# Optimization experiments

Measured on AMD Instinct MI355X. Metric: run time of the kernel, lower is better.

Reference implementation:

```python
import jax, jax.numpy as jnp
import numpy as np

N = 100000      # nodes
E = 1600000     # edges
G = 4096        # graphs (molecules)
F_NODE, F_MOL = 64, 128
EN, D0, D1, D2, D3, OUT = 64, 128, 128, 256, 64, 1
EPS_BN = 1e-5


def setup_inputs() -> dict:
    key = jax.random.key(0)
    ks = iter(jax.random.split(key, 40))
    def w(shape, scale=0.1):
        return jax.random.normal(next(ks), shape, dtype=jnp.float32) * scale
    inp = {
        "x": jax.random.normal(next(ks), (N, F_NODE), dtype=jnp.float32),
        "atom_ens": jax.random.uniform(next(ks), (N,), dtype=jnp.float32),
        "mol_feats": jax.random.normal(next(ks), (G, F_MOL), dtype=jnp.float32),
        "edge_index": jax.random.randint(next(ks), (2, E), 0, N, dtype=jnp.int32),
        "batch": jnp.sort(jax.random.randint(next(ks), (N,), 0, G, dtype=jnp.int32)),
        # electronegativity embedding
        "W_en": w((F_NODE, EN)), "b_en": w((EN,)),
        # GCN layers
        "gW0": w((EN, D0)), "gb0": w((D0,)),
        "gW1": w((D0, D0)), "gb1": w((D0,)),
        "gW2": w((D0, D1)), "gb2": w((D1,)),
        "bn_gc_g": jnp.ones((D0,), jnp.float32), "bn_gc_b": jnp.zeros((D0,), jnp.float32),
        # mol-feature MLP branch
        "mW0": w((F_MOL, D0)), "mb0": w((D0,)),
        "mW1": w((D0, D0)), "mb1": w((D0,)),
        "mW2": w((D0, D1)), "mb2": w((D1,)),
        "bn_m_g": jnp.ones((D0,), jnp.float32), "bn_m_b": jnp.zeros((D0,), jnp.float32),
        # fused head
        "fW0": w((2 * D1, D2)), "fb0": w((D2,)),
        "fW1": w((D2, D2)), "fb1": w((D2,)),
        "fW2": w((D2, D3)), "fb2": w((D3,)),
        "fW3": w((D3, OUT)), "fb3": w((OUT,)),
    }
    return inp


def _bn(x, gamma, beta):
    # BatchNorm1d in training mode: batch stats, biased variance
    mu = jnp.mean(x, axis=0)
    var = jnp.mean(jnp.square(x - mu), axis=0)
    return (x - mu) * jax.lax.rsqrt(var + EPS_BN) * gamma + beta


def reference(x, atom_ens, mol_feats, edge_index, batch,
              W_en, b_en,
              gW0, gb0, gW1, gb1, gW2, gb2, bn_gc_g, bn_gc_b,
              mW0, mb0, mW1, mb1, mW2, mb2, bn_m_g, bn_m_b,
              fW0, fb0, fW1, fb1, fW2, fb2, fW3, fb3):
    silu = jax.nn.silu
    # GCN normalization with self-loops (PyG gcn_norm), shared by all layers
    loop = jnp.arange(N, dtype=edge_index.dtype)
    src = jnp.concatenate([edge_index[0], loop])   # [E+N]
    dst = jnp.concatenate([edge_index[1], loop])
    deg = jax.ops.segment_sum(jnp.ones_like(dst, x.dtype), dst, num_segments=N)
    dinv = jax.lax.rsqrt(deg)                      # deg >= 1 due to self-loops
    norm = dinv[src] * dinv[dst]                   # [E+N]

    def gcn(h, W, b):
        h = h @ W                                  # transform then propagate
        msg = h[src] * norm[:, None]               # gather + scale
        return jax.ops.segment_sum(msg, dst, num_segments=N) + b

    # calc_en: linear -> L2 normalize per node -> scale by atom electronegativity
    fo = x @ W_en + b_en
    fo = fo / jnp.maximum(jnp.linalg.norm(fo, axis=1, keepdims=True), 1e-12)
    en = atom_ens[:, None] * fo

    h = silu(_bn(gcn(en, gW0, gb0), bn_gc_g, bn_gc_b))
    h = silu(gcn(h, gW1, gb1))
    h = silu(gcn(h, gW2, gb2))
    hg = jax.ops.segment_sum(h, batch, num_segments=G)   # global_add_pool

    hm = silu(_bn(mol_feats @ mW0 + mb0, bn_m_g, bn_m_b))
    hm = silu(hm @ mW1 + mb1)
    hm = silu(hm @ mW2 + mb2)

    hg = jnp.concatenate([hg, hm], axis=1)
    hg = silu(hg @ fW0 + fb0)
    hg = silu(hg @ fW1 + fb1)
    hg = silu(hg @ fW2 + fb2)
    return hg @ fW3 + fb3
```

## Files before the change

### kernel.cpp

```cpp
#include <hip/hip_runtime.h>
#include <math.h>

static __device__ __forceinline__ float silu_f(float v){ return v/(1.0f+expf(-v)); }
static __device__ __forceinline__ unsigned short f2bf(float f){
  unsigned int u=__float_as_uint(f);
  unsigned int r=(u + 0x7fffu + ((u>>16)&1u))>>16;
  return (unsigned short)r;
}
static __device__ __forceinline__ void bf2f(unsigned int u, float& a, float& b){
  a=__uint_as_float(u<<16); b=__uint_as_float(u & 0xffff0000u);
}

__global__ void k_hist(const int* __restrict__ dst, int* __restrict__ cnt, int E){
  int e = blockIdx.x*256+threadIdx.x;
  if(e<E) atomicAdd(&cnt[dst[e]],1);
}
__global__ void k_dinv(const int* __restrict__ cnt, float* __restrict__ dinv, int n){
  int i = blockIdx.x*256+threadIdx.x;
  if(i<n) dinv[i]=rsqrtf((float)(cnt[i]+1));
}
__global__ void k_scan1(const int* __restrict__ cnt, int* __restrict__ rp, int* __restrict__ bs, int n){
  __shared__ int sh[256];
  int tid=threadIdx.x;
  int base = blockIdx.x*1024 + tid*4;
  int v0=0,v1=0,v2=0,v3=0;
  if(base+0<n)v0=cnt[base+0];
  if(base+1<n)v1=cnt[base+1];
  if(base+2<n)v2=cnt[base+2];
  if(base+3<n)v3=cnt[base+3];
  int s=v0+v1+v2+v3;
  sh[tid]=s; __syncthreads();
  for(int off=1;off<256;off<<=1){
    int t = (tid>=off)? sh[tid-off] : 0;
    __syncthreads();
    sh[tid]+=t;
    __syncthreads();
  }
  int run = sh[tid]-s;
  if(tid==255) bs[blockIdx.x]=sh[255];
  if(base+0<n){rp[base+0]=run; run+=v0;}
  if(base+1<n){rp[base+1]=run; run+=v1;}
  if(base+2<n){rp[base+2]=run; run+=v2;}
  if(base+3<n){rp[base+3]=run; run+=v3;}
}
__global__ void k_scan2(int* bs, int nb, int* rp, int n){
  __shared__ int sh[256];
  int tid=threadIdx.x;
  int v = (tid<nb)? bs[tid] : 0;
  sh[tid]=v; __syncthreads();
  for(int off=1;off<256;off<<=1){
    int t=(tid>=off)?sh[tid-off]:0;
    __syncthreads();
    sh[tid]+=t;
    __syncthreads();
  }
  if(tid<nb) bs[tid]=sh[tid]-v;
  if(tid==255) rp[n]=sh[255];
}
__global__ void k_scan3(int* rp, const int* __restrict__ bs, int n){
  int i = blockIdx.x*256+threadIdx.x;
  if(i<n) rp[i]+=bs[i>>10];
}
__global__ void k_fill(const int* __restrict__ src, const int* __restrict__ dst, int* cur,
                       const int* __restrict__ rp, int* __restrict__ csr, int E){
  int e = blockIdx.x*256+threadIdx.x;
  if(e<E){ int d=dst[e]; int p=atomicAdd(&cur[d],1); csr[rp[d]+p]=src[e]; }
}

__global__ __launch_bounds__(256) void k_en(const float* __restrict__ x, const float* __restrict__ W,
    const float* __restrict__ b, const float* __restrict__ ae, unsigned short* __restrict__ out, int Nn){
  __shared__ float As[32][68];
  __shared__ float Bs[32][68];
  int bm = blockIdx.x*64;
  int tid = threadIdx.x;
  int ty = tid/16, tx = tid%16;
  float acc[4][4] = {{0}};
  for(int k0=0;k0<64;k0+=32){
    #pragma unroll
    for(int i=0;i<8;i++){
      int idx = i*256+tid;
      int r = idx>>5, c = idx&31;
      As[c][r] = (bm+r<Nn) ? x[(size_t)(bm+r)*64 + k0+c] : 0.0f;
    }
    #pragma unroll
    for(int i=0;i<8;i++){
      int idx = i*256+tid;
      int r = idx>>6, c = idx&63;
      Bs[r][c] = W[(size_t)(k0+r)*64 + c];
    }
    __syncthreads();
    #pragma unroll
    for(int k=0;k<32;k++){
      float a0=As[k][ty*4+0],a1=As[k][ty*4+1],a2=As[k][ty*4+2],a3=As[k][ty*4+3];
      float b0=Bs[k][tx*4+0],b1=Bs[k][tx*4+1],b2=Bs[k][tx*4+2],b3=Bs[k][tx*4+3];
      acc[0][0]+=a0*b0; acc[0][1]+=a0*b1; acc[0][2]+=a0*b2; acc[0][3]+=a0*b3;
      acc[1][0]+=a1*b0; acc[1][1]+=a1*b1; acc[1][2]+=a1*b2; acc[1][3]+=a1*b3;
      acc[2][0]+=a2*b0; acc[2][1]+=a2*b1; acc[2][2]+=a2*b2; acc[2][3]+=a2*b3;
      acc[3][0]+=a3*b0; acc[3][1]+=a3*b1; acc[3][2]+=a3*b2; acc[3][3]+=a3*b3;
    }
    __syncthreads();
  }
  float bb0=b[tx*4+0], bb1=b[tx*4+1], bb2=b[tx*4+2], bb3=b[tx*4+3];
  #pragma unroll
  for(int i=0;i<4;i++){
    int row = bm+ty*4+i;
    float v0=acc[i][0]+bb0, v1=acc[i][1]+bb1, v2=acc[i][2]+bb2, v3=acc[i][3]+bb3;
    float ss = v0*v0+v1*v1+v2*v2+v3*v3;
    ss += __shfl_xor(ss,1); ss += __shfl_xor(ss,2);
    ss += __shfl_xor(ss,4); ss += __shfl_xor(ss,8);
    if(row<Nn){
      float scale = ae[row] / fmaxf(sqrtf(ss), 1e-12f);
      ushort4 o;
      o.x=f2bf(v0*scale); o.y=f2bf(v1*scale); o.z=f2bf(v2*scale); o.w=f2bf(v3*scale);
      *(ushort4*)&out[(size_t)row*64 + tx*4] = o;
    }
  }
}

template<int FB>
__global__ __launch_bounds__(256) void k_prop_bf(const unsigned short* __restrict__ h, float* __restrict__ out,
                       const int* __restrict__ rp, const int* __restrict__ csr,
                       const float* __restrict__ dinv, int Nn){
  int t = blockIdx.x*256+threadIdx.x;
  int n = t/FB;
  if(n>=Nn) return;
  int g = (t%FB)*8;
  const int F = FB*8;
  float dn = dinv[n];
  float a0,a1,a2,a3,a4,a5,a6,a7;
  {
    uint4 u = *(const uint4*)&h[(size_t)n*F+g];
    bf2f(u.x,a0,a1); bf2f(u.y,a2,a3); bf2f(u.z,a4,a5); bf2f(u.w,a6,a7);
    a0*=dn;a1*=dn;a2*=dn;a3*=dn;a4*=dn;a5*=dn;a6*=dn;a7*=dn;
  }
  int e=rp[n], e1=rp[n+1];
  for(; e+1<e1; e+=2){
    int s0=csr[e], s1=csr[e+1];
    float w0=dinv[s0], w1=dinv[s1];
    uint4 u0 = *(const uint4*)&h[(size_t)s0*F+g];
    uint4 u1 = *(const uint4*)&h[(size_t)s1*F+g];
    float b0,b1,b2,b3,b4,b5,b6,b7;
    bf2f(u0.x,b0,b1); bf2f(u0.y,b2,b3); bf2f(u0.z,b4,b5); bf2f(u0.w,b6,b7);
    a0+=b0*w0; a1+=b1*w0; a2+=b2*w0; a3+=b3*w0;
    a4+=b4*w0; a5+=b5*w0; a6+=b6*w0; a7+=b7*w0;
    bf2f(u1.x,b0,b1); bf2f(u1.y,b2,b3); bf2f(u1.z,b4,b5); bf2f(u1.w,b6,b7);
    a0+=b0*w1; a1+=b1*w1; a2+=b2*w1; a3+=b3*w1;
    a4+=b4*w1; a5+=b5*w1; a6+=b6*w1; a7+=b7*w1;
  }
  if(e<e1){
    int s=csr[e]; float w=dinv[s];
    uint4 u = *(const uint4*)&h[(size_t)s*F+g];
    float b0,b1,b2,b3,b4,b5,b6,b7;
    bf2f(u.x,b0,b1); bf2f(u.y,b2,b3); bf2f(u.z,b4,b5); bf2f(u.w,b6,b7);
    a0+=b0*w; a1+=b1*w; a2+=b2*w; a3+=b3*w;
    a4+=b4*w; a5+=b5*w; a6+=b6*w; a7+=b7*w;
  }
  float4 o0; o0.x=a0*dn; o0.y=a1*dn; o0.z=a2*dn; o0.w=a3*dn;
  float4 o1; o1.x=a4*dn; o1.y=a5*dn; o1.z=a6*dn; o1.w=a7*dn;
  *(float4*)&out[(size_t)n*F+g]   = o0;
  *(float4*)&out[(size_t)n*F+g+4] = o1;
}

__global__ __launch_bounds__(256) void k_gemm(const float* __restrict__ A, const float* __restrict__ W,
    const float* __restrict__ bias, float* __restrict__ C, unsigned short* __restrict__ Cbf,
    int M, int K, int D, int ldc, int act){
  __shared__ float As[32][68];
  __shared__ float Bs[32][68];
  int bm = blockIdx.x*64, bn = blockIdx.y*64;
  int tid = threadIdx.x;
  int ty = tid/16, tx = tid%16;
  float acc[4][4] = {{0}};
  for(int k0=0;k0<K;k0+=32){
    #pragma unroll
    for(int i=0;i<8;i++){
      int idx = i*256+tid;
      int r = idx>>5, c = idx&31;
      As[c][r] = (bm+r<M) ? A[(size_t)(bm+r)*K + k0+c] : 0.0f;
    }
    #pragma unroll
    for(int i=0;i<8;i++){
      int idx = i*256+tid;
      int r = idx>>6, c = idx&63;
      Bs[r][c] = W[(size_t)(k0+r)*D + bn+c];
    }
    __syncthreads();
    #pragma unroll
    for(int k=0;k<32;k++){
      float a0=As[k][ty*4+0],a1=As[k][ty*4+1],a2=As[k][ty*4+2],a3=As[k][ty*4+3];
      float b0=Bs[k][tx*4+0],b1=Bs[k][tx*4+1],b2=Bs[k][tx*4+2],b3=Bs[k][tx*4+3];
      acc[0][0]+=a0*b0; acc[0][1]+=a0*b1; acc[0][2]+=a0*b2; acc[0][3]+=a0*b3;
      acc[1][0]+=a1*b0; acc[1][1]+=a1*b1; acc[1][2]+=a1*b2; acc[1][3]+=a1*b3;
      acc[2][0]+=a2*b0; acc[2][1]+=a2*b1; acc[2][2]+=a2*b2; acc[2][3]+=a2*b3;
      acc[3][0]+=a3*b0; acc[3][1]+=a3*b1; acc[3][2]+=a3*b2; acc[3][3]+=a3*b3;
    }
    __syncthreads();
  }
  #pragma unroll
  for(int i=0;i<4;i++){
    int r = bm+ty*4+i;
    if(r<M){
      #pragma unroll
      for(int j=0;j<4;j++){
        int c = bn+tx*4+j;
        float v = acc[i][j] + bias[c];
        if(act) v = silu_f(v);
        if(C)   C[(size_t)r*ldc + c] = v;
        if(Cbf) Cbf[(size_t)r*ldc + c] = f2bf(v);
      }
    }
  }
}

__global__ __launch_bounds__(256) void k_bnstats(const float* __restrict__ A, float* __restrict__ sums,
                                                 int rows, int rpb){
  __shared__ float sh1[4][128];
  __shared__ float sh2[4][128];
  int tid=threadIdx.x;
  int sub=tid>>5;
  int cg=tid&31;
  int r0=blockIdx.x*rpb, r1=min(r0+rpb,rows);
  float s1x=0,s1y=0,s1z=0,s1w=0, s2x=0,s2y=0,s2z=0,s2w=0;
  for(int r=r0+sub; r<r1; r+=8){
    float4 v = *(const float4*)&A[(size_t)r*128 + cg*4];
    s1x+=v.x; s2x+=v.x*v.x;
    s1y+=v.y; s2y+=v.y*v.y;
    s1z+=v.z; s2z+=v.z*v.z;
    s1w+=v.w; s2w+=v.w*v.w;
  }
  s1x+=__shfl_xor(s1x,32); s1y+=__shfl_xor(s1y,32); s1z+=__shfl_xor(s1z,32); s1w+=__shfl_xor(s1w,32);
  s2x+=__shfl_xor(s2x,32); s2y+=__shfl_xor(s2y,32); s2z+=__shfl_xor(s2z,32); s2w+=__shfl_xor(s2w,32);
  int wave=tid>>6, lane=tid&63;
  if(lane<32){
    sh1[wave][cg*4+0]=s1x; sh1[wave][cg*4+1]=s1y; sh1[wave][cg*4+2]=s1z; sh1[wave][cg*4+3]=s1w;
    sh2[wave][cg*4+0]=s2x; sh2[wave][cg*4+1]=s2y; sh2[wave][cg*4+2]=s2z; sh2[wave][cg*4+3]=s2w;
  }
  __syncthreads();
  if(tid<128){
    float p=sh1[0][tid]+sh1[1][tid]+sh1[2][tid]+sh1[3][tid];
    atomicAdd(&sums[tid],p);
  } else {
    int c=tid-128;
    float p=sh2[0][c]+sh2[1][c]+sh2[2][c]+sh2[3][c];
    atomicAdd(&sums[128+c],p);
  }
}
__global__ void k_bnfinal(const float* __restrict__ sums, const float* __restrict__ g,
                          const float* __restrict__ b, float* __restrict__ sc, int rows){
  int c = threadIdx.x;
  float mu = sums[c]/rows;
  float var = sums[128+c]/rows - mu*mu;
  float a = g[c]*rsqrtf(var+1e-5f);
  sc[c]=a; sc[128+c]=b[c]-mu*a;
}
__global__ __launch_bounds__(256) void k_bnsilu_bf(const float* __restrict__ A, unsigned short* __restrict__ O,
                                                   const float* __restrict__ sc, int total4){
  int i = blockIdx.x*256+threadIdx.x;
  if(i<total4){
    int c4=(i&31)*4;
    float4 v = ((const float4*)A)[i];
    ushort4 o;
    o.x = f2bf(silu_f(v.x*sc[c4+0]+sc[128+c4+0]));
    o.y = f2bf(silu_f(v.y*sc[c4+1]+sc[128+c4+1]));
    o.z = f2bf(silu_f(v.z*sc[c4+2]+sc[128+c4+2]));
    o.w = f2bf(silu_f(v.w*sc[c4+3]+sc[128+c4+3]));
    *(ushort4*)&O[(size_t)i*4] = o;
  }
}
__global__ __launch_bounds__(256) void k_bnsilu(float* __restrict__ A, const float* __restrict__ sc, int total4){
  int i = blockIdx.x*256+threadIdx.x;
  if(i<total4){
    int c4=(i&31)*4;
    float4 v = ((const float4*)A)[i];
    v.x = silu_f(v.x*sc[c4+0]+sc[128+c4+0]);
    v.y = silu_f(v.y*sc[c4+1]+sc[128+c4+1]);
    v.z = silu_f(v.z*sc[c4+2]+sc[128+c4+2]);
    v.w = silu_f(v.w*sc[c4+3]+sc[128+c4+3]);
    ((float4*)A)[i] = v;
  }
}

__global__ __launch_bounds__(256) void k_pool(const float* __restrict__ h, const int* __restrict__ batch,
                       float* __restrict__ P, int Nn, int G){
  int t = blockIdx.x*256+threadIdx.x;
  int g = t>>5;
  if(g>=G) return;
  int c4=(t&31)*4;
  int lo=0, hi=Nn;
  while(lo<hi){ int m=(lo+hi)>>1; if(batch[m]<g) lo=m+1; else hi=m; }
  int s=lo;
  lo=0; hi=Nn;
  while(lo<hi){ int m=(lo+hi)>>1; if(batch[m]<=g) lo=m+1; else hi=m; }
  int e=lo;
  float ax=0,ay=0,az=0,aw=0;
  for(int r=s;r<e;r++){
    float4 v = *(const float4*)&h[(size_t)r*128+c4];
    ax+=v.x; ay+=v.y; az+=v.z; aw+=v.w;
  }
  float4 o; o.x=ax;o.y=ay;o.z=az;o.w=aw;
  *(float4*)&P[(size_t)g*256+c4] = o;
}

__global__ void k_dot(const float* __restrict__ z, const float* __restrict__ w,
                      const float* __restrict__ b, float* __restrict__ out){
  int g = blockIdx.x; int lane = threadIdx.x;
  float p = z[(size_t)g*64+lane]*w[lane];
  #pragma unroll
  for(int off=32;off;off>>=1) p += __shfl_xor(p,off);
  if(lane==0) out[g] = p + b[0];
}

extern "C" void kernel_launch(void* const* d_in, const int* in_sizes, int n_in,
                              void* d_out, int out_size, void* d_ws, size_t ws_size,
                              hipStream_t stream){
  const float* x       =(const float*)d_in[0];
  const float* atom_ens=(const float*)d_in[1];
  const float* mol     =(const float*)d_in[2];
  const int*   eidx    =(const int*)d_in[3];
  const int*   batch   =(const int*)d_in[4];
  const float* W_en=(const float*)d_in[5];  const float* b_en=(const float*)d_in[6];
  const float* gW0=(const float*)d_in[7];   const float* gb0=(const float*)d_in[8];
  const float* gW1=(const float*)d_in[9];   const float* gb1=(const float*)d_in[10];
  const float* gW2=(const float*)d_in[11];  const float* gb2=(const float*)d_in[12];
  const float* bn_gc_g=(const float*)d_in[13]; const float* bn_gc_b=(const float*)d_in[14];
  const float* mW0=(const float*)d_in[15];  const float* mb0=(const float*)d_in[16];
  const float* mW1=(const float*)d_in[17];  const float* mb1=(const float*)d_in[18];
  const float* mW2=(const float*)d_in[19];  const float* mb2=(const float*)d_in[20];
  const float* bn_m_g=(const float*)d_in[21]; const float* bn_m_b=(const float*)d_in[22];
  const float* fW0=(const float*)d_in[23];  const float* fb0=(const float*)d_in[24];
  const float* fW1=(const float*)d_in[25];  const float* fb1=(const float*)d_in[26];
  const float* fW2=(const float*)d_in[27];  const float* fb2=(const float*)d_in[28];
  const float* fW3=(const float*)d_in[29];  const float* fb3=(const float*)d_in[30];

  const int N = in_sizes[1];
  const int E = in_sizes[3]/2;
  const int G = in_sizes[2]/128;
  const int* esrc = eidx;
  const int* edst = eidx+E;

  char* ws=(char*)d_ws;
  size_t o=0;
  float* A=(float*)(ws+o);    o += (size_t)N*128*4;
  float* B=(float*)(ws+o);    o += (size_t)N*128*4;
  unsigned short* Abf=(unsigned short*)(ws+o); o += (size_t)N*128*2;
  float* dinv=(float*)(ws+o); o += (size_t)N*4;
  int* cnt=(int*)(ws+o);      o += (size_t)N*4;
  int* rp=(int*)(ws+o);       o += (size_t)(N+1)*4; o=(o+255)&~(size_t)255;
  int* bs=(int*)(ws+o);       o += 4096;
  float* sums=(float*)(ws+o); o += 1024;
  float* sc=(float*)(ws+o);   o += 1024;
  int* csr=(int*)(ws+o);      o += (size_t)E*4;
  if(o > ws_size) return;

  unsigned short* enbf = (unsigned short*)A;
  float* P  = B;
  float* Q  = P + (size_t)G*256;
  float* MB0= Q + (size_t)G*256;
  float* MB1= MB0 + (size_t)G*128;
  float* Z2 = MB1 + (size_t)G*128;

  dim3 blk256(256);
  int nb = (N+1023)/1024;

  hipMemsetAsync(cnt, 0, (size_t)N*4, stream);
  k_hist<<<dim3((E+255)/256), blk256, 0, stream>>>(edst, cnt, E);
  k_dinv<<<dim3((N+255)/256), blk256, 0, stream>>>(cnt, dinv, N);
  k_scan1<<<dim3(nb), blk256, 0, stream>>>(cnt, rp, bs, N);
  k_scan2<<<dim3(1), blk256, 0, stream>>>(bs, nb, rp, N);
  k_scan3<<<dim3((N+255)/256), blk256, 0, stream>>>(rp, bs, N);
  hipMemsetAsync(cnt, 0, (size_t)N*4, stream);
  k_fill<<<dim3((E+255)/256), blk256, 0, stream>>>(esrc, edst, cnt, rp, csr, E);

  k_en<<<dim3((N+63)/64), blk256, 0, stream>>>(x, W_en, b_en, atom_ens, enbf, N);

  k_prop_bf<8><<<dim3((N*8+255)/256), blk256, 0, stream>>>(enbf, B, rp, csr, dinv, N);
  k_gemm<<<dim3((N+63)/64, 2), blk256, 0, stream>>>(B, gW0, gb0, A, (unsigned short*)nullptr, N, 64, 128, 128, 0);
  {
    int nblk=512, rpb=(N+nblk-1)/nblk;
    hipMemsetAsync(sums, 0, 1024, stream);
    k_bnstats<<<dim3(nblk), blk256, 0, stream>>>(A, sums, N, rpb);
    k_bnfinal<<<dim3(1), dim3(128), 0, stream>>>(sums, bn_gc_g, bn_gc_b, sc, N);
    k_bnsilu_bf<<<dim3((N*32+255)/256), blk256, 0, stream>>>(A, Abf, sc, N*32);
  }

  k_prop_bf<16><<<dim3((N*16+255)/256), blk256, 0, stream>>>(Abf, B, rp, csr, dinv, N);
  k_gemm<<<dim3((N+63)/64, 2), blk256, 0, stream>>>(B, gW1, gb1, (float*)nullptr, Abf, N, 128, 128, 128, 1);

  k_prop_bf<16><<<dim3((N*16+255)/256), blk256, 0, stream>>>(Abf, B, rp, csr, dinv, N);
  k_gemm<<<dim3((N+63)/64, 2), blk256, 0, stream>>>(B, gW2, gb2, A, (unsigned short*)nullptr, N, 128, 128, 128, 1);

  k_pool<<<dim3((G*32+255)/256), blk256, 0, stream>>>(A, batch, P, N, G);

  k_gemm<<<dim3((G+63)/64, 2), blk256, 0, stream>>>(mol, mW0, mb0, MB0, (unsigned short*)nullptr, G, 128, 128, 128, 0);
  {
    int nblk=64, rpb=(G+nblk-1)/nblk;
    hipMemsetAsync(sums, 0, 1024, stream);
    k_bnstats<<<dim3(nblk), blk256, 0, stream>>>(MB0, sums, G, rpb);
    k_bnfinal<<<dim3(1), dim3(128), 0, stream>>>(sums, bn_m_g, bn_m_b, sc, G);
    k_bnsilu<<<dim3((G*32+255)/256), blk256, 0, stream>>>(MB0, sc, G*32);
  }
  k_gemm<<<dim3((G+63)/64, 2), blk256, 0, stream>>>(MB0, mW1, mb1, MB1, (unsigned short*)nullptr, G, 128, 128, 128, 1);
  k_gemm<<<dim3((G+63)/64, 2), blk256, 0, stream>>>(MB1, mW2, mb2, P+128, (unsigned short*)nullptr, G, 128, 128, 256, 1);

  k_gemm<<<dim3((G+63)/64, 4), blk256, 0, stream>>>(P, fW0, fb0, Q, (unsigned short*)nullptr, G, 256, 256, 256, 1);
  k_gemm<<<dim3((G+63)/64, 4), blk256, 0, stream>>>(Q, fW1, fb1, P, (unsigned short*)nullptr, G, 256, 256, 256, 1);
  k_gemm<<<dim3((G+63)/64, 1), blk256, 0, stream>>>(P, fW2, fb2, Z2, (unsigned short*)nullptr, G, 256, 64, 64, 1);
  k_dot<<<dim3(G), dim3(64), 0, stream>>>(Z2, fW3, fb3, (float*)d_out);
}
```

Before: 895.5 us.

## Build CSR via two-level bucketed counting sort with block-local atomics

Replaces the per-node global histogram, three-pass scan and per-node atomic fill with a two-level scheme. Edges are bucketed by destination/128 using global atomics on about 782 counters, and each bucket is then sorted locally in shared memory, which also yields row pointers and dinv. This cuts the global atomic traffic spread across 100k counters and removes several launches, but global atomics now contend on far fewer addresses, and the extra pass writes and reads an int2 pairs buffer that reuses the A workspace.

```diff
diff --git a/kernel.cpp b/kernel.cpp
--- a/kernel.cpp
+++ b/kernel.cpp
@@ -11,60 +11,68 @@
   a=__uint_as_float(u<<16); b=__uint_as_float(u & 0xffff0000u);
 }
 
-__global__ void k_hist(const int* __restrict__ dst, int* __restrict__ cnt, int E){
+__global__ void kb_hist(const int* __restrict__ dst, int* __restrict__ bhist, int E){
   int e = blockIdx.x*256+threadIdx.x;
-  if(e<E) atomicAdd(&cnt[dst[e]],1);
-}
-__global__ void k_dinv(const int* __restrict__ cnt, float* __restrict__ dinv, int n){
-  int i = blockIdx.x*256+threadIdx.x;
-  if(i<n) dinv[i]=rsqrtf((float)(cnt[i]+1));
-}
-__global__ void k_scan1(const int* __restrict__ cnt, int* __restrict__ rp, int* __restrict__ bs, int n){
-  __shared__ int sh[256];
+  if(e<E) atomicAdd(&bhist[dst[e]>>7],1);
+}
+__global__ __launch_bounds__(1024) void kb_scan(const int* __restrict__ bhist, int* __restrict__ boff,
+                       int* __restrict__ bcur, int* __restrict__ rp, int B, int Nn){
+  __shared__ int sh[1024];
   int tid=threadIdx.x;
-  int base = blockIdx.x*1024 + tid*4;
-  int v0=0,v1=0,v2=0,v3=0;
-  if(base+0<n)v0=cnt[base+0];
-  if(base+1<n)v1=cnt[base+1];
-  if(base+2<n)v2=cnt[base+2];
-  if(base+3<n)v3=cnt[base+3];
-  int s=v0+v1+v2+v3;
-  sh[tid]=s; __syncthreads();
-  for(int off=1;off<256;off<<=1){
+  int v = (tid<B)? bhist[tid] : 0;
+  sh[tid]=v; __syncthreads();
+  for(int off=1;off<1024;off<<=1){
     int t = (tid>=off)? sh[tid-off] : 0;
     __syncthreads();
     sh[tid]+=t;
     __syncthreads();
   }
-  int run = sh[tid]-s;
-  if(tid==255) bs[blockIdx.x]=sh[255];
-  if(base+0<n){rp[base+0]=run; run+=v0;}
-  if(base+1<n){rp[base+1]=run; run+=v1;}
-  if(base+2<n){rp[base+2]=run; run+=v2;}
-  if(base+3<n){rp[base+3]=run; run+=v3;}
-}
-__global__ void k_scan2(int* bs, int nb, int* rp, int n){
-  __shared__ int sh[256];
-  int tid=threadIdx.x;
-  int v = (tid<nb)? bs[tid] : 0;
-  sh[tid]=v; __syncthreads();
-  for(int off=1;off<256;off<<=1){
-    int t=(tid>=off)?sh[tid-off]:0;
-    __syncthreads();
-    sh[tid]+=t;
-    __syncthreads();
-  }
-  if(tid<nb) bs[tid]=sh[tid]-v;
-  if(tid==255) rp[n]=sh[255];
-}
-__global__ void k_scan3(int* rp, const int* __restrict__ bs, int n){
-  int i = blockIdx.x*256+threadIdx.x;
-  if(i<n) rp[i]+=bs[i>>10];
-}
-__global__ void k_fill(const int* __restrict__ src, const int* __restrict__ dst, int* cur,
-                       const int* __restrict__ rp, int* __restrict__ csr, int E){
+  if(tid<B){ int ex=sh[tid]-v; boff[tid]=ex; bcur[tid]=ex; }
+  if(tid==1023){ boff[B]=sh[1023]; rp[Nn]=sh[1023]; }
+}
+__global__ void kb_fill(const int* __restrict__ src, const int* __restrict__ dst,
+                        int* __restrict__ bcur, int2* __restrict__ pairs, int E){
   int e = blockIdx.x*256+threadIdx.x;
-  if(e<E){ int d=dst[e]; int p=atomicAdd(&cur[d],1); csr[rp[d]+p]=src[e]; }
+  if(e<E){
+    int s=src[e], d=dst[e];
+    int p=atomicAdd(&bcur[d>>7],1);
+    pairs[p]=make_int2(s,d);
+  }
+}
+__global__ __launch_bounds__(256) void k_node(const int2* __restrict__ pairs, const int* __restrict__ boff,
+                       int* __restrict__ rp, float* __restrict__ dinv, int* __restrict__ csr, int Nn){
+  __shared__ int lcnt[128], lscan[128], lcur[128];
+  int b = blockIdx.x;
+  int tid = threadIdx.x;
+  int base = b<<7;
+  int seg0 = boff[b], seg1 = boff[b+1];
+  if(tid<128) lcnt[tid]=0;
+  __syncthreads();
+  for(int i=seg0+tid; i<seg1; i+=256) atomicAdd(&lcnt[pairs[i].y & 127],1);
+  __syncthreads();
+  if(tid<128) lscan[tid]=lcnt[tid];
+  __syncthreads();
+  for(int off=1;off<128;off<<=1){
+    int t = (tid<128 && tid>=off)? lscan[tid-off] : 0;
+    __syncthreads();
+    if(tid<128) lscan[tid]+=t;
+    __syncthreads();
+  }
+  if(tid<128){
+    int ex = lscan[tid]-lcnt[tid];
+    lcur[tid]=ex;
+    int node = base+tid;
+    if(node<Nn){
+      rp[node] = seg0+ex;
+      dinv[node] = rsqrtf((float)(lcnt[tid]+1));
+    }
+  }
+  __syncthreads();
+  for(int i=seg0+tid; i<seg1; i+=256){
+    int2 pr = pairs[i];
+    int p = atomicAdd(&lcur[pr.y & 127],1);
+    csr[seg0+p] = pr.x;
+  }
 }
 
 __global__ __launch_bounds__(256) void k_en(const float* __restrict__ x, const float* __restrict__ W,
@@ -334,46 +342,45 @@
   const int N = in_sizes[1];
   const int E = in_sizes[3]/2;
   const int G = in_sizes[2]/128;
+  const int B = (N+127)>>7;
   const int* esrc = eidx;
   const int* edst = eidx+E;
 
   char* ws=(char*)d_ws;
   size_t o=0;
   float* A=(float*)(ws+o);    o += (size_t)N*128*4;
-  float* B=(float*)(ws+o);    o += (size_t)N*128*4;
+  float* Bbuf=(float*)(ws+o); o += (size_t)N*128*4;
   unsigned short* Abf=(unsigned short*)(ws+o); o += (size_t)N*128*2;
   float* dinv=(float*)(ws+o); o += (size_t)N*4;
-  int* cnt=(int*)(ws+o);      o += (size_t)N*4;
   int* rp=(int*)(ws+o);       o += (size_t)(N+1)*4; o=(o+255)&~(size_t)255;
-  int* bs=(int*)(ws+o);       o += 4096;
+  int* bhist=(int*)(ws+o);    o += (size_t)(B+1)*4;
+  int* boff=(int*)(ws+o);     o += (size_t)(B+1)*4;
+  int* bcur=(int*)(ws+o);     o += (size_t)(B+1)*4; o=(o+255)&~(size_t)255;
   float* sums=(float*)(ws+o); o += 1024;
   float* sc=(float*)(ws+o);   o += 1024;
   int* csr=(int*)(ws+o);      o += (size_t)E*4;
   if(o > ws_size) return;
 
+  int2* pairs = (int2*)A;
   unsigned short* enbf = (unsigned short*)A;
-  float* P  = B;
+  float* P  = Bbuf;
   float* Q  = P + (size_t)G*256;
   float* MB0= Q + (size_t)G*256;
   float* MB1= MB0 + (size_t)G*128;
   float* Z2 = MB1 + (size_t)G*128;
 
   dim3 blk256(256);
-  int nb = (N+1023)/1024;
-
-  hipMemsetAsync(cnt, 0, (size_t)N*4, stream);
-  k_hist<<<dim3((E+255)/256), blk256, 0, stream>>>(edst, cnt, E);
-  k_dinv<<<dim3((N+255)/256), blk256, 0, stream>>>(cnt, dinv, N);
-  k_scan1<<<dim3(nb), blk256, 0, stream>>>(cnt, rp, bs, N);
-  k_scan2<<<dim3(1), blk256, 0, stream>>>(bs, nb, rp, N);
-  k_scan3<<<dim3((N+255)/256), blk256, 0, stream>>>(rp, bs, N);
-  hipMemsetAsync(cnt, 0, (size_t)N*4, stream);
-  k_fill<<<dim3((E+255)/256), blk256, 0, stream>>>(esrc, edst, cnt, rp, csr, E);
+
+  hipMemsetAsync(bhist, 0, (size_t)(B+1)*4, stream);
+  kb_hist<<<dim3((E+255)/256), blk256, 0, stream>>>(edst, bhist, E);
+  kb_scan<<<dim3(1), dim3(1024), 0, stream>>>(bhist, boff, bcur, rp, B, N);
+  kb_fill<<<dim3((E+255)/256), blk256, 0, stream>>>(esrc, edst, bcur, pairs, E);
+  k_node<<<dim3(B), blk256, 0, stream>>>(pairs, boff, rp, dinv, csr, N);
 
   k_en<<<dim3((N+63)/64), blk256, 0, stream>>>(x, W_en, b_en, atom_ens, enbf, N);
 
-  k_prop_bf<8><<<dim3((N*8+255)/256), blk256, 0, stream>>>(enbf, B, rp, csr, dinv, N);
-  k_gemm<<<dim3((N+63)/64, 2), blk256, 0, stream>>>(B, gW0, gb0, A, (unsigned short*)nullptr, N, 64, 128, 128, 0);
+  k_prop_bf<8><<<dim3((N*8+255)/256), blk256, 0, stream>>>(enbf, Bbuf, rp, csr, dinv, N);
+  k_gemm<<<dim3((N+63)/64, 2), blk256, 0, stream>>>(Bbuf, gW0, gb0, A, (unsigned short*)nullptr, N, 64, 128, 128, 0);
   {
     int nblk=512, rpb=(N+nblk-1)/nblk;
     hipMemsetAsync(sums, 0, 1024, stream);
@@ -382,11 +389,11 @@
     k_bnsilu_bf<<<dim3((N*32+255)/256), blk256, 0, stream>>>(A, Abf, sc, N*32);
   }
 
-  k_prop_bf<16><<<dim3((N*16+255)/256), blk256, 0, stream>>>(Abf, B, rp, csr, dinv, N);
-  k_gemm<<<dim3((N+63)/64, 2), blk256, 0, stream>>>(B, gW1, gb1, (float*)nullptr, Abf, N, 128, 128, 128, 1);
-
-  k_prop_bf<16><<<dim3((N*16+255)/256), blk256, 0, stream>>>(Abf, B, rp, csr, dinv, N);
-  k_gemm<<<dim3((N+63)/64, 2), blk256, 0, stream>>>(B, gW2, gb2, A, (unsigned short*)nullptr, N, 128, 128, 128, 1);
+  k_prop_bf<16><<<dim3((N*16+255)/256), blk256, 0, stream>>>(Abf, Bbuf, rp, csr, dinv, N);
+  k_gemm<<<dim3((N+63)/64, 2), blk256, 0, stream>>>(Bbuf, gW1, gb1, (float*)nullptr, Abf, N, 128, 128, 128, 1);
+
+  k_prop_bf<16><<<dim3((N*16+255)/256), blk256, 0, stream>>>(Abf, Bbuf, rp, csr, dinv, N);
+  k_gemm<<<dim3((N+63)/64, 2), blk256, 0, stream>>>(Bbuf, gW2, gb2, A, (unsigned short*)nullptr, N, 128, 128, 128, 1);
 
   k_pool<<<dim3((G*32+255)/256), blk256, 0, stream>>>(A, batch, P, N, G);
 
```

Result: slower. 1.497 ms (+67.2%).
